# Kernel optimization log

Measured on AMD Instinct MI355X. Metric: run time of the kernel, lower is better.

The kernel has to match this reference:

```python
import jax, jax.numpy as jnp
import numpy as np

N = 8192   # num_neurons
P = 64     # num stored patterns


def setup_inputs() -> dict:
    key = jax.random.key(0)
    k1, k2 = jax.random.split(key)
    # Bipolar (+/-1) stored patterns, as in classical Hopfield usage
    X = jnp.where(jax.random.normal(k1, (N, P)) >= 0, 1.0, -1.0).astype(jnp.float32)
    # Initial (possibly corrupted) bipolar state
    state = jnp.where(jax.random.normal(k2, (N,)) >= 0, 1.0, -1.0).astype(jnp.float32)
    # Visit order for asynchronous updates (torch.randperm in original; any permutation is valid)
    perm = jnp.arange(N, dtype=jnp.int32)
    return {"X": X, "state": state, "perm": perm}


def reference(X, state, perm):
    n = X.shape[0]
    # W = X X^T / N with zero diagonal (Hebbian weights), as in __init__
    W = (X @ X.T) / n                                  # [N, N]
    W = W * (1.0 - jnp.eye(n, dtype=W.dtype))
    # Strictly sequential asynchronous update over the given permutation
    def step(s, i):
        act = jnp.dot(W[i], s)                         # dot(W[i], new_state)
        s = s.at[i].set(jnp.where(act >= 0, 1.0, -1.0).astype(s.dtype))
        return s, None
    final_state, _ = jax.lax.scan(step, state, perm)
    return final_state
```

## Files before the change

### kernel.cpp

```cpp
#include <hip/hip_runtime.h>
#include <stdint.h>


#define NB 128
typedef unsigned long long u64;
typedef unsigned u32;


__device__ __forceinline__ void glds16(const void* g, void* l) {
  __builtin_amdgcn_global_load_lds(
      (const __attribute__((address_space(1))) void*)g,
      (__attribute__((address_space(3))) void*)l, 16, 0, 0);
}

__global__ __launch_bounds__(256) void hop_prep(
    const float* __restrict__ X, const float* __restrict__ state,
    const int* __restrict__ perm, float* __restrict__ m0,
    float* __restrict__ Ysw, u64* __restrict__ sig, u64* __restrict__ sigT,
    float* __restrict__ sps)
{
  const int b = blockIdx.x, t = threadIdx.x;
  const int wv = t >> 6, ln = t & 63;
  __shared__ u64 sigL[64];
  __shared__ float red[4][64];

  float acc = 0.f;
  #pragma unroll
  for (int jj = 0; jj < 16; ++jj) {
    const int j = wv*16 + jj;
    const int r = perm[b*64 + j];
    const float sr = state[r];
    const float x = X[(size_t)r*64 + ln];
    Ysw[(size_t)b*4096 + j*64 + ((((ln >> 2) ^ (j & 7)) << 2) | (ln & 3))] = x * sr;
    u64 bb = __ballot(x < 0.f);
    if (sr < 0.f) bb = ~bb;
    if (ln == 0) { sig[b*64 + j] = bb; sigL[j] = bb; }
    acc = fmaf(x, sr, acc);
  }
  red[wv][ln] = acc;
  __syncthreads();

  {
    const u64 gs = sigL[ln];
    #pragma unroll
    for (int jj = 0; jj < 16; ++jj) {
      const int p = wv*16 + jj;
      u64 tb = __ballot((unsigned)((gs >> p) & 1ull));
      if (ln == 0) sigT[b*64 + p] = tb;
    }
  }

  if (t < 64) {
    atomicAdd(&m0[t], (red[0][t] + red[1][t]) + (red[2][t] + red[3][t]));
    sps[b*64 + t] = state[perm[b*64 + t]];
  }
}

__device__ __forceinline__ int corr_term(u32 slo, u32 shi, int i) {
  const u32 a = (u32)__builtin_amdgcn_readlane((int)slo, i);
  const u32 b = (u32)__builtin_amdgcn_readlane((int)shi, i);
  return __popc(slo ^ a) + __popc(shi ^ b);
}

__device__ __forceinline__ void process_block(
    const float* __restrict__ Yc, const u64 sg, const u64 st,
    const int rr, const float ss, float* mlds, float& mreg,
    float* __restrict__ out, const int lane, const int ybase, const int lswz)
{
  float q0=0.f,q1=0.f,q2=0.f,q3=0.f;
  const float4* mv4 = (const float4*)mlds;
  #pragma unroll
  for (int g = 0; g < 16; ++g) {
    const float4 yv = *(const float4*)&Yc[ybase + ((g ^ lswz) << 2)];
    const float4 mv = mv4[g];
    q0 = fmaf(yv.x, mv.x, q0); q1 = fmaf(yv.y, mv.y, q1);
    q2 = fmaf(yv.z, mv.z, q2); q3 = fmaf(yv.w, mv.w, q3);
  }
  const int U0 = (((int)((q0+q1)+(q2+q3))) << 1) - ((ss < 0.f) ? 1 : 0) - 128;
  const u32 slo = (u32)sg, shi = (u32)(sg >> 32);

  u64 F = __ballot(U0 < 0);
  u64 flips = 0ull;
  if (F) {
    int Ub = U0;
    {
      int acc0 = 0, acc1 = 0;
      u64 rem = F;
      while (rem) {
        const int i = (int)__builtin_ctzll(rem); rem &= rem - 1ull;
        const int pc = corr_term(slo, shi, i);
        acc0 += (lane > i) ? pc : 0;
        if (rem) {
          const int i2 = (int)__builtin_ctzll(rem); rem &= rem - 1ull;
          const int pc2 = corr_term(slo, shi, i2);
          acc1 += (lane > i2) ? pc2 : 0;
        }
      }
      const int cnt = (int)__builtin_amdgcn_mbcnt_hi(
          (u32)(F >> 32), __builtin_amdgcn_mbcnt_lo((u32)F, 0u));
      Ub += ((acc0 + acc1) << 3) - (cnt << 8);
    }
    bool conv = false;
    for (int it = 0; it < 6; ++it) {
      const u64 Fn = __ballot(Ub < 0);
      if (Fn == F) { conv = true; break; }
      u64 dd = Fn ^ F;
      while (dd) {
        const int i = (int)__builtin_ctzll(dd); dd &= dd - 1ull;
        const int pc8 = (corr_term(slo, shi, i) << 3) - 256;
        const int d = ((Fn >> i) & 1ull) ? pc8 : -pc8;
        Ub += (lane > i) ? d : 0;
      }
      F = Fn;
    }
    if (conv) {
      flips = F;
    } else {
      int Us = U0;
      u64 live = ~0ull;
      u64 mm = __ballot(Us < 0);
      while (mm) {
        const int i = (int)__builtin_ctzll(mm);
        flips |= (1ull << i);
        live = (i < 63) ? ((~0ull) << (i + 1)) : 0ull;
        Us += (corr_term(slo, shi, i) << 3) - 256;
        mm = __ballot(Us < 0) & live;
      }
    }
  }

  if (flips) {
    const int nf = (int)__popcll(flips);
    const int pc = (int)__popcll(flips & st);
    mreg += (float)(4*pc - 2*nf);
    mlds[lane] = mreg;
  }
  out[rr] = ((flips >> lane) & 1ull) ? -ss : ss;
}

#define PREFETCH(BN, BUF, sg, st, rr, ss) {                                   \
  const float* ys = Ysw + (size_t)(BN)*4096 + lane*4;                         \
  _Pragma("unroll")                                                           \
  for (int it = 0; it < 16; ++it) glds16(ys + it*256, &(BUF)[it*256]);        \
  sg = sig[(BN)*64+lane]; st = sigT[(BN)*64+lane];                            \
  rr = perm[(BN)*64+lane]; ss = sps[(BN)*64+lane];                            \
}

__global__ __launch_bounds__(64) void hop_solve(
    const int* __restrict__ perm, const float* __restrict__ m0,
    const float* __restrict__ Ysw, const u64* __restrict__ sig,
    const u64* __restrict__ sigT, const float* __restrict__ sps,
    float* __restrict__ out)
{
  __shared__ __align__(16) float mlds[64];
  __shared__ __align__(16) float Ybuf[2][4096];
  const int lane = threadIdx.x;
  const int ybase = lane*64, lswz = lane & 7;

  float mreg = m0[lane];
  mlds[lane] = mreg;

  u64 sgA, stA, sgB, stB; int rA, rB; float sA, sB;
  PREFETCH(0, Ybuf[0], sgA, stA, rA, sA);
  asm volatile("s_waitcnt vmcnt(0)" ::: "memory");

  for (int bb = 0; bb < NB; bb += 2) {
    PREFETCH(bb+1, Ybuf[1], sgB, stB, rB, sB);
    process_block(Ybuf[0], sgA, stA, rA, sA, mlds, mreg, out, lane, ybase, lswz);
    asm volatile("s_waitcnt vmcnt(1)" ::: "memory");
    if (bb + 2 < NB) PREFETCH(bb+2, Ybuf[0], sgA, stA, rA, sA);
    process_block(Ybuf[1], sgB, stB, rB, sB, mlds, mreg, out, lane, ybase, lswz);
    asm volatile("s_waitcnt vmcnt(1)" ::: "memory");
  }
}

extern "C" void kernel_launch(void* const* d_in, const int* in_sizes, int n_in,
                              void* d_out, int out_size, void* d_ws, size_t ws_size,
                              hipStream_t stream) {
  const float* X     = (const float*)d_in[0];
  const float* state = (const float*)d_in[1];
  const int*   perm  = (const int*)d_in[2];
  float* outp = (float*)d_out;

  float* m0  = (float*)d_ws;
  float* Ysw = m0 + 64;
  u64*   sig = (u64*)(Ysw + 128*4096);
  u64*   sigT= sig + 8192;
  float* sps = (float*)(sigT + 8192);

  hipMemsetAsync(m0, 0, 64*sizeof(float), stream);
  hop_prep<<<dim3(NB), dim3(256), 0, stream>>>(X, state, perm, m0, Ysw, sig, sigT, sps);
  hop_solve<<<dim3(1), dim3(64), 0, stream>>>(perm, m0, Ysw, sig, sigT, sps, outp);
}
```

Baseline: 385.5 us.

## Split sequential solve across two ping-ponging waves with cross-block correction

The single-wave solve loop is replaced by two wavefronts that alternate ownership of 64-row blocks. While one wave resolves the flips of block b, the other has already computed its block's matvec against a stale magnetization and corrects it with a popcount sweep over block b's flips. This is meant to take the 64-wide matvec and the LDS staging off the serial critical path. In exchange it adds a workgroup barrier per block and the extra xsweep work.

After: 449.9 us. 1.17x slower.

```diff
diff --git a/kernel.cpp b/kernel.cpp
--- a/kernel.cpp
+++ b/kernel.cpp
@@ -62,115 +62,155 @@
   return __popc(slo ^ a) + __popc(shi ^ b);
 }
 
-__device__ __forceinline__ void process_block(
-    const float* __restrict__ Yc, const u64 sg, const u64 st,
-    const int rr, const float ss, float* mlds, float& mreg,
-    float* __restrict__ out, const int lane, const int ybase, const int lswz)
-{
+__device__ __forceinline__ u64 resolve64(const int U0, const u64 sg, const int lane) {
+  const u32 slo = (u32)sg, shi = (u32)(sg >> 32);
+  u64 F = __ballot(U0 < 0);
+  if (!F) return 0ull;
+  int Ub = U0;
+  {
+    int a0 = 0, a1 = 0;
+    u64 rem = F;
+    while (rem) {
+      const int i = (int)__builtin_ctzll(rem); rem &= rem - 1ull;
+      const int pc = corr_term(slo, shi, i);
+      a0 += (lane > i) ? pc : 0;
+      if (rem) {
+        const int i2 = (int)__builtin_ctzll(rem); rem &= rem - 1ull;
+        const int pc2 = corr_term(slo, shi, i2);
+        a1 += (lane > i2) ? pc2 : 0;
+      }
+    }
+    const int cnt = (int)__builtin_amdgcn_mbcnt_hi(
+        (u32)(F >> 32), __builtin_amdgcn_mbcnt_lo((u32)F, 0u));
+    Ub += ((a0 + a1) << 3) - (cnt << 8);
+  }
+  bool conv = false;
+  for (int it = 0; it < 6; ++it) {
+    const u64 Fn = __ballot(Ub < 0);
+    if (Fn == F) { conv = true; break; }
+    u64 dd = Fn ^ F;
+    while (dd) {
+      const int i = (int)__builtin_ctzll(dd); dd &= dd - 1ull;
+      const int pc8 = (corr_term(slo, shi, i) << 3) - 256;
+      const int d = ((Fn >> i) & 1ull) ? pc8 : -pc8;
+      Ub += (lane > i) ? d : 0;
+    }
+    F = Fn;
+  }
+  if (conv) return F;
+  u64 flips = 0ull, live = ~0ull;
+  int Us = U0;
+  u64 mm = __ballot(Us < 0);
+  while (mm) {
+    const int i = (int)__builtin_ctzll(mm);
+    flips |= (1ull << i);
+    live = (i < 63) ? ((~0ull) << (i + 1)) : 0ull;
+    Us += (corr_term(slo, shi, i) << 3) - 256;
+    mm = __ballot(Us < 0) & live;
+  }
+  return flips;
+}
+
+__device__ __forceinline__ int xsweep(const u64 fb, const u64 sigPrev, const u64 sigOwn) {
+  const u32 plo = (u32)sigPrev, phi = (u32)(sigPrev >> 32);
+  const u32 olo = (u32)sigOwn,  ohi = (u32)(sigOwn >> 32);
+  int a0 = 0, a1 = 0;
+  u64 rem = fb;
+  while (rem) {
+    const int i = (int)__builtin_ctzll(rem); rem &= rem - 1ull;
+    a0 += __popc(olo ^ (u32)__builtin_amdgcn_readlane((int)plo, i))
+        + __popc(ohi ^ (u32)__builtin_amdgcn_readlane((int)phi, i));
+    if (rem) {
+      const int i2 = (int)__builtin_ctzll(rem); rem &= rem - 1ull;
+      a1 += __popc(olo ^ (u32)__builtin_amdgcn_readlane((int)plo, i2))
+          + __popc(ohi ^ (u32)__builtin_amdgcn_readlane((int)phi, i2));
+    }
+  }
+  const int nf = (int)__popcll(fb);
+  return ((a0 + a1) << 3) - (nf << 8);
+}
+
+__device__ __forceinline__ int matvec_q(const float* __restrict__ Yl,
+                                        const float* __restrict__ mb,
+                                        const int ybase, const int lswz) {
   float q0=0.f,q1=0.f,q2=0.f,q3=0.f;
-  const float4* mv4 = (const float4*)mlds;
+  const float4* mv4 = (const float4*)mb;
   #pragma unroll
   for (int g = 0; g < 16; ++g) {
-    const float4 yv = *(const float4*)&Yc[ybase + ((g ^ lswz) << 2)];
+    const float4 yv = *(const float4*)&Yl[ybase + ((g ^ lswz) << 2)];
     const float4 mv = mv4[g];
     q0 = fmaf(yv.x, mv.x, q0); q1 = fmaf(yv.y, mv.y, q1);
     q2 = fmaf(yv.z, mv.z, q2); q3 = fmaf(yv.w, mv.w, q3);
   }
-  const int U0 = (((int)((q0+q1)+(q2+q3))) << 1) - ((ss < 0.f) ? 1 : 0) - 128;
-  const u32 slo = (u32)sg, shi = (u32)(sg >> 32);
-
-  u64 F = __ballot(U0 < 0);
-  u64 flips = 0ull;
-  if (F) {
-    int Ub = U0;
-    {
-      int acc0 = 0, acc1 = 0;
-      u64 rem = F;
-      while (rem) {
-        const int i = (int)__builtin_ctzll(rem); rem &= rem - 1ull;
-        const int pc = corr_term(slo, shi, i);
-        acc0 += (lane > i) ? pc : 0;
-        if (rem) {
-          const int i2 = (int)__builtin_ctzll(rem); rem &= rem - 1ull;
-          const int pc2 = corr_term(slo, shi, i2);
-          acc1 += (lane > i2) ? pc2 : 0;
-        }
-      }
-      const int cnt = (int)__builtin_amdgcn_mbcnt_hi(
-          (u32)(F >> 32), __builtin_amdgcn_mbcnt_lo((u32)F, 0u));
-      Ub += ((acc0 + acc1) << 3) - (cnt << 8);
-    }
-    bool conv = false;
-    for (int it = 0; it < 6; ++it) {
-      const u64 Fn = __ballot(Ub < 0);
-      if (Fn == F) { conv = true; break; }
-      u64 dd = Fn ^ F;
-      while (dd) {
-        const int i = (int)__builtin_ctzll(dd); dd &= dd - 1ull;
-        const int pc8 = (corr_term(slo, shi, i) << 3) - 256;
-        const int d = ((Fn >> i) & 1ull) ? pc8 : -pc8;
-        Ub += (lane > i) ? d : 0;
-      }
-      F = Fn;
-    }
-    if (conv) {
-      flips = F;
-    } else {
-      int Us = U0;
-      u64 live = ~0ull;
-      u64 mm = __ballot(Us < 0);
-      while (mm) {
-        const int i = (int)__builtin_ctzll(mm);
-        flips |= (1ull << i);
-        live = (i < 63) ? ((~0ull) << (i + 1)) : 0ull;
-        Us += (corr_term(slo, shi, i) << 3) - 256;
-        mm = __ballot(Us < 0) & live;
-      }
-    }
-  }
-
-  if (flips) {
-    const int nf = (int)__popcll(flips);
-    const int pc = (int)__popcll(flips & st);
-    mreg += (float)(4*pc - 2*nf);
-    mlds[lane] = mreg;
-  }
-  out[rr] = ((flips >> lane) & 1ull) ? -ss : ss;
-}
-
-#define PREFETCH(BN, BUF, sg, st, rr, ss) {                                   \
-  const float* ys = Ysw + (size_t)(BN)*4096 + lane*4;                         \
-  _Pragma("unroll")                                                           \
-  for (int it = 0; it < 16; ++it) glds16(ys + it*256, &(BUF)[it*256]);        \
-  sg = sig[(BN)*64+lane]; st = sigT[(BN)*64+lane];                            \
-  rr = perm[(BN)*64+lane]; ss = sps[(BN)*64+lane];                            \
-}
-
-__global__ __launch_bounds__(64) void hop_solve(
+  return (int)((q0+q1)+(q2+q3));
+}
+
+__device__ __forceinline__ void stageTo(float* __restrict__ buf,
+                                        const float* __restrict__ ys) {
+  #pragma unroll
+  for (int it = 0; it < 16; ++it) glds16(ys + it*256, buf + it*256);
+}
+
+__global__ __launch_bounds__(128) void hop_solve(
     const int* __restrict__ perm, const float* __restrict__ m0,
     const float* __restrict__ Ysw, const u64* __restrict__ sig,
     const u64* __restrict__ sigT, const float* __restrict__ sps,
     float* __restrict__ out)
 {
-  __shared__ __align__(16) float mlds[64];
   __shared__ __align__(16) float Ybuf[2][4096];
-  const int lane = threadIdx.x;
+  __shared__ float mlds[2][64];
+  __shared__ u64 fl_lds[4];
+  const int tid = threadIdx.x;
+  const int wid = tid >> 6, lane = tid & 63;
   const int ybase = lane*64, lswz = lane & 7;
 
   float mreg = m0[lane];
-  mlds[lane] = mreg;
-
-  u64 sgA, stA, sgB, stB; int rA, rB; float sA, sB;
-  PREFETCH(0, Ybuf[0], sgA, stA, rA, sA);
+  mlds[wid][lane] = mreg;
+
+  stageTo(Ybuf[wid], Ysw + (size_t)wid*4096 + lane*4);
+  u64 sgOwn = sig[wid*64 + lane];
+  int rOwn  = perm[wid*64 + lane];
+  float sOwn = sps[wid*64 + lane];
+  u64 sgCur = sig[lane];
+  u64 stCur = sigT[lane];
   asm volatile("s_waitcnt vmcnt(0)" ::: "memory");
-
-  for (int bb = 0; bb < NB; bb += 2) {
-    PREFETCH(bb+1, Ybuf[1], sgB, stB, rB, sB);
-    process_block(Ybuf[0], sgA, stA, rA, sA, mlds, mreg, out, lane, ybase, lswz);
-    asm volatile("s_waitcnt vmcnt(1)" ::: "memory");
-    if (bb + 2 < NB) PREFETCH(bb+2, Ybuf[0], sgA, stA, rA, sA);
-    process_block(Ybuf[1], sgB, stB, rB, sB, mlds, mreg, out, lane, ybase, lswz);
-    asm volatile("s_waitcnt vmcnt(1)" ::: "memory");
+  int U = (matvec_q(Ybuf[wid], mlds[wid], ybase, lswz) << 1)
+          - ((sOwn < 0.f) ? 1 : 0) - 128;
+  asm volatile("s_waitcnt lgkmcnt(0)" ::: "memory");
+  stageTo(Ybuf[wid], Ysw + (size_t)(wid+2)*4096 + lane*4);
+
+  for (int b = 0; b < NB; ++b) {
+    const bool owner = ((b & 1) == wid);
+    if (owner) {
+      const u64 flips = resolve64(U, sgOwn, lane);
+      out[rOwn] = ((flips >> lane) & 1ull) ? -sOwn : sOwn;
+      if (lane == 0) fl_lds[b & 3] = flips;
+    }
+    __syncthreads();
+    const u64 fb = fl_lds[b & 3];
+    {
+      const int nf = (int)__popcll(fb);
+      const int pc = (int)__popcll(fb & stCur);
+      mreg += (float)(4*pc - 2*nf);
+    }
+    u64 sgN = 0, stN = 0;
+    if (b + 1 < NB) { sgN = sig[(b+1)*64 + lane]; stN = sigT[(b+1)*64 + lane]; }
+    if (!owner) {
+      if (b + 1 < NB) U += xsweep(fb, sgCur, sgOwn);
+    } else {
+      if (b + 2 < NB) {
+        mlds[wid][lane] = mreg;
+        asm volatile("s_waitcnt vmcnt(0)" ::: "memory");
+        const int q = matvec_q(Ybuf[wid], mlds[wid], ybase, lswz);
+        asm volatile("s_waitcnt lgkmcnt(0)" ::: "memory");
+        if (b + 4 < NB) stageTo(Ybuf[wid], Ysw + (size_t)(b+4)*4096 + lane*4);
+        sgOwn = sig[(b+2)*64 + lane];
+        rOwn  = perm[(b+2)*64 + lane];
+        sOwn  = sps[(b+2)*64 + lane];
+        U = (q << 1) - ((sOwn < 0.f) ? 1 : 0) - 128;
+      }
+    }
+    sgCur = sgN; stCur = stN;
   }
 }
 
@@ -190,5 +230,5 @@
 
   hipMemsetAsync(m0, 0, 64*sizeof(float), stream);
   hop_prep<<<dim3(NB), dim3(256), 0, stream>>>(X, state, perm, m0, Ysw, sig, sigT, sps);
-  hop_solve<<<dim3(1), dim3(64), 0, stream>>>(perm, m0, Ysw, sig, sigT, sps, outp);
-}
+  hop_solve<<<dim3(1), dim3(128), 0, stream>>>(perm, m0, Ysw, sig, sigT, sps, outp);
+}
```
